# Performance work log

Measured on AMD Instinct MI355X. Metric: run time of the kernel, lower is better.

## Reference

```python
import jax, jax.numpy as jnp
import numpy as np

NUM_CLASSES = 1      # hard-coded in panoptic_inference2
MASK_THR = 1e-3      # cur_masks[:, k] >= 0.001


def _panoptic_single(logits, mask_logits, pad):
    # logits: [Q, C+1], mask_logits: [P, Q], pad: [P] bool (all False here)
    scores = logits.max(axis=-1)                      # cur_scores per query
    labels = jnp.argmax(logits, axis=-1)              # predicted class per query
    keep = labels != NUM_CLASSES                      # drop 'no-object' queries

    m = jax.nn.sigmoid(mask_logits)                   # [P, Q] cur_masks
    prob_masks = scores[None, :] * m                  # cur_prob_masks [P, Q]
    # emulate column selection cur_masks[:, keep] by masking with -inf
    masked = jnp.where(keep[None, :], prob_masks, -jnp.inf)

    # probabilities = softmax over (kept) queries; max_confs = per-point max prob
    soft = jax.nn.softmax(masked, axis=1)             # [P, Q]
    max_confs = soft.max(axis=1)                      # [P]

    # cur_mask_ids = argmax over kept queries (indices in full query space)
    mid = jnp.argmax(masked, axis=1)                  # [P]
    m_sel = jnp.take_along_axis(m, mid[:, None], axis=1)[:, 0]
    # point contributes to segment k iff argmax==k AND sigmoid>=thr (and not padded)
    valid = (m_sel >= MASK_THR) & (~pad) & keep[mid]  # [P]

    Q = logits.shape[0]
    # per-query area of mask = (mid==k) & thr ; segment kept iff nonempty
    counts = jnp.zeros((Q,), jnp.int32).at[mid].add(valid.astype(jnp.int32))
    nonempty = counts > 0
    # sequential segment ids in query order (masks are disjoint, so the
    # conf-based reordering in the original cannot change sem/ins)
    seg_id = jnp.cumsum(nonempty.astype(jnp.int32))   # [Q]

    ins = jnp.where(valid, seg_id[mid], 0).astype(jnp.int32)
    sem = jnp.where(valid, labels[mid].astype(jnp.int32), 0)
    return sem, ins, max_confs


def setup_inputs() -> dict:
    key = jax.random.key(0)
    k1, k2 = jax.random.split(key)
    B, P, Q, C1 = 2, 200000, 100, NUM_CLASSES + 1
    pred_logits = jax.random.normal(k1, (B, Q, C1), dtype=jnp.float32)
    pred_masks = jax.random.normal(k2, (B, P, Q), dtype=jnp.float32)
    padding = jnp.zeros((B, P), dtype=bool)
    return {"pred_logits": pred_logits, "pred_masks": pred_masks, "padding": padding}


def reference(pred_logits, pred_masks, padding):
    sem, ins, max_confs = jax.vmap(_panoptic_single)(pred_logits, pred_masks, padding)
    return sem, ins, max_confs
```

## Files before the change

kernel.cpp:

```cpp
#include <hip/hip_runtime.h>
#include <math.h>

#define B_   2
#define P_   200000
#define Q_   100
#define NBLK 3125


__global__ void pano_prep(const float* __restrict__ logits,
                          float* __restrict__ msc)
{
    const int b = blockIdx.x, tid = threadIdx.x;
    if (tid < Q_) {
        float l0 = logits[(b * Q_ + tid) * 2 + 0];
        float l1 = logits[(b * Q_ + tid) * 2 + 1];
        msc[b * Q_ + tid] = (l1 > l0) ? -1e30f : fmaxf(l0, l1);
    }
}

__global__ __launch_bounds__(256) void pano_pass1(
    const float* __restrict__ masks,
    const unsigned char* __restrict__ pad,
    float* __restrict__ out,
    const float* __restrict__ msc,
    ulonglong2* __restrict__ flags)
{
    const int b = blockIdx.y, tid = threadIdx.x;
    __shared__ float s_msc[Q_];
    __shared__ int   s_flag[Q_];
    if (tid < Q_) { s_msc[tid] = msc[b * Q_ + tid]; s_flag[tid] = 0; }
    __syncthreads();

    const int wave = tid >> 6, wl = tid & 63;
    const int g = wl >> 2, l = wl & 3;
    const int p = blockIdx.x * 64 + wave * 16 + g;

    const float* rowp = masks + ((size_t)b * P_ + p) * Q_;
    const float4* grow = reinterpret_cast<const float4*>(rowp);

    float4 v[7];
    #pragma unroll
    for (int k = 0; k < 6; ++k) v[k] = grow[k * 4 + l];
    v[6] = grow[24];

    float S0 = 0.0f;
    float v1 = -INFINITY, v2 = -INFINITY, m1 = 0.0f;
    int   q1 = -1;

    #pragma unroll
    for (int k = 0; k < 7; ++k) {
        const bool act = (k < 6) || (l == 0);
        const int  qb  = (k < 6) ? (16 * k + 4 * l) : 96;
        float xv[4] = {v[k].x, v[k].y, v[k].z, v[k].w};
        #pragma unroll
        for (int e = 0; e < 4; ++e) {
            int q = qb + e;
            float m   = __builtin_amdgcn_rcpf(1.0f + __expf(-xv[e]));
            float val = act ? s_msc[q] * m : -INFINITY;
            S0 += __expf(val);
            bool t = val > v1;
            v2 = t ? v1 : fmaxf(v2, val);
            v1 = t ? val : v1;
            m1 = t ? m   : m1;
            q1 = t ? q   : q1;
        }
    }

    #pragma unroll
    for (int off = 1; off <= 2; off <<= 1) {
        float So  = __shfl_xor(S0, off, 64);
        float v1o = __shfl_xor(v1, off, 64);
        float v2o = __shfl_xor(v2, off, 64);
        float m1o = __shfl_xor(m1, off, 64);
        int   q1o = __shfl_xor(q1, off, 64);
        S0 += So;
        bool t = (v1o > v1) || (v1o == v1 && (unsigned)q1o < (unsigned)q1);
        v2 = fmaxf(fminf(v1, v1o), fmaxf(v2, v2o));
        v1 = t ? v1o : v1;
        m1 = t ? m1o : m1;
        q1 = t ? q1o : q1;
    }

    if (l == 0 && (v1 - v2) < 5e-5f) {
        float bv = -INFINITY, bm = 0.0f; int bq = -1;
        for (int q = 0; q < Q_; ++q) {
            float x = rowp[q];
            float e = expf(-x);
            float m = 1.0f / (1.0f + e);
            float vv = s_msc[q] * m;
            if (vv > bv) { bv = vv; bq = q; bm = m; }
        }
        q1 = bq; m1 = bm;
    }

    bool valid = (q1 >= 0) && (s_msc[q1] > -1e29f) &&
                 (m1 >= 1e-3f) &&
                 (pad[(size_t)b * P_ + p] == 0);

    float conf = __expf(v1) * __builtin_amdgcn_rcpf(S0);
    float insf = valid ? (float)q1 : -1.0f;
    if (l == 0 && valid) s_flag[q1] = 1;

    int   src    = (wl & 15) * 4;
    float conf_g = __shfl(conf, src, 64);
    float insf_g = __shfl(insf, src, 64);
    if (wl < 16) {
        int prow = blockIdx.x * 64 + wave * 16 + wl;
        size_t o = (size_t)b * P_ + prow;
        out[o]                       = 0.0f;
        out[(size_t)B_ * P_ + o]     = insf_g;
        out[2 * (size_t)B_ * P_ + o] = conf_g;
    }

    __syncthreads();
    {
        bool f = (tid < Q_) ? (s_flag[tid] != 0) : false;
        unsigned long long m = __ballot(f);
        if (tid == 0)  flags[b * NBLK + blockIdx.x].x = m;
        if (tid == 64) flags[b * NBLK + blockIdx.x].y = m;
    }
}

__global__ __launch_bounds__(256) void pano_pass2(
    const ulonglong2* __restrict__ flags,
    int* __restrict__ seg)
{
    const int b = blockIdx.x, tid = threadIdx.x;
    unsigned long long m0 = 0ull, m1 = 0ull;
    for (int i = tid; i < NBLK; i += 256) {
        ulonglong2 w = flags[b * NBLK + i];
        m0 |= w.x; m1 |= w.y;
    }
    #pragma unroll
    for (int off = 32; off; off >>= 1) {
        m0 |= __shfl_xor(m0, off, 64);
        m1 |= __shfl_xor(m1, off, 64);
    }
    __shared__ unsigned long long sm0[4], sm1[4];
    if ((tid & 63) == 0) { sm0[tid >> 6] = m0; sm1[tid >> 6] = m1; }
    __syncthreads();
    if (tid == 0) {
        m0 = sm0[0] | sm0[1] | sm0[2] | sm0[3];
        m1 = sm1[0] | sm1[1] | sm1[2] | sm1[3];
        int c = 0;
        for (int q = 0; q < Q_; ++q) {
            c += (int)((q < 64 ? (m0 >> q) : (m1 >> (q - 64))) & 1ull);
            seg[b * Q_ + q] = c;
        }
    }
}

__global__ __launch_bounds__(256) void pano_pass3(
    const int* __restrict__ seg,
    float* __restrict__ out)
{
    const int b = blockIdx.y, tid = threadIdx.x;
    __shared__ int s_seg[Q_];
    if (tid < Q_) s_seg[tid] = seg[b * Q_ + tid];
    __syncthreads();

    int p = blockIdx.x * blockDim.x + tid;
    if (p < P_) {
        size_t o = (size_t)B_ * P_ + (size_t)b * P_ + p;
        float f = out[o];
        out[o] = (f >= 0.0f) ? (float)s_seg[(int)f] : 0.0f;
    }
}

extern "C" void kernel_launch(void* const* d_in, const int* in_sizes, int n_in,
                              void* d_out, int out_size, void* d_ws, size_t ws_size,
                              hipStream_t stream) {
    const float* logits = (const float*)d_in[0];
    const float* masks  = (const float*)d_in[1];
    const unsigned char* pad = (const unsigned char*)d_in[2];
    float* out = (float*)d_out;

    ulonglong2* flags = (ulonglong2*)d_ws;
    float*      mscp  = (float*)((char*)d_ws + 102400);
    int*        seg   = (int*)((char*)d_ws + 103424);

    pano_prep<<<dim3(B_), dim3(128), 0, stream>>>(logits, mscp);

    dim3 block(256);
    pano_pass1<<<dim3(NBLK, B_), block, 0, stream>>>(masks, pad, out, mscp, flags);
    pano_pass2<<<dim3(B_), block, 0, stream>>>(flags, seg);
    pano_pass3<<<dim3((P_ + 255) / 256, B_), block, 0, stream>>>(seg, out);
}
```

Measured before the change: 245.4 us.

## Persistent grid-stride pass1 with register prefetch and fused prep/pass2 kernels

Pass1 now runs a fixed grid of 512 blocks per batch that loop over row tiles, double-buffering the next tile's mask loads in registers while the current tile is computed. The logits prep kernel is folded into pass1's shared-memory setup. The segment-id scan (pass2) is folded into every pass3 block, which now reduces only 512 flag words per batch. Together these cut launch count and flag traffic and aim to hide load latency. The cost is higher register pressure from prefetch buffers and redundant scan work in each pass3 block.

```diff
diff --git a/kernel.cpp b/kernel.cpp
--- a/kernel.cpp
+++ b/kernel.cpp
@@ -4,131 +4,153 @@
 #define B_   2
 #define P_   200000
 #define Q_   100
-#define NBLK 3125
+#define NIT  3125
+#define GX   512
 
 
-__global__ void pano_prep(const float* __restrict__ logits,
-                          float* __restrict__ msc)
-{
-    const int b = blockIdx.x, tid = threadIdx.x;
-    if (tid < Q_) {
-        float l0 = logits[(b * Q_ + tid) * 2 + 0];
-        float l1 = logits[(b * Q_ + tid) * 2 + 1];
-        msc[b * Q_ + tid] = (l1 > l0) ? -1e30f : fmaxf(l0, l1);
-    }
-}
-
 __global__ __launch_bounds__(256) void pano_pass1(
+    const float* __restrict__ logits,
     const float* __restrict__ masks,
     const unsigned char* __restrict__ pad,
     float* __restrict__ out,
-    const float* __restrict__ msc,
     ulonglong2* __restrict__ flags)
 {
     const int b = blockIdx.y, tid = threadIdx.x;
     __shared__ float s_msc[Q_];
     __shared__ int   s_flag[Q_];
-    if (tid < Q_) { s_msc[tid] = msc[b * Q_ + tid]; s_flag[tid] = 0; }
+    if (tid < Q_) {
+        float l0 = logits[(b * Q_ + tid) * 2 + 0];
+        float l1 = logits[(b * Q_ + tid) * 2 + 1];
+        s_msc[tid]  = (l1 > l0) ? -1e30f : fmaxf(l0, l1);
+        s_flag[tid] = 0;
+    }
     __syncthreads();
 
-    const int wave = tid >> 6, wl = tid & 63;
-    const int g = wl >> 2, l = wl & 3;
-    const int p = blockIdx.x * 64 + wave * 16 + g;
+    const int wave  = tid >> 6, wl = tid & 63;
+    const int g     = wl >> 2,  l  = wl & 3;
+    const int rbase = wave * 16 + g;
 
-    const float* rowp = masks + ((size_t)b * P_ + p) * Q_;
-    const float4* grow = reinterpret_cast<const float4*>(rowp);
+    const float* mbase = masks + (size_t)b * P_ * Q_;
 
-    float4 v[7];
-    #pragma unroll
-    for (int k = 0; k < 6; ++k) v[k] = grow[k * 4 + l];
-    v[6] = grow[24];
-
-    float S0 = 0.0f;
-    float v1 = -INFINITY, v2 = -INFINITY, m1 = 0.0f;
-    int   q1 = -1;
-
-    #pragma unroll
-    for (int k = 0; k < 7; ++k) {
-        const bool act = (k < 6) || (l == 0);
-        const int  qb  = (k < 6) ? (16 * k + 4 * l) : 96;
-        float xv[4] = {v[k].x, v[k].y, v[k].z, v[k].w};
+    float4 v[7], vn[7];
+    int it = blockIdx.x;
+    {
+        const float4* grow =
+            (const float4*)(mbase + ((size_t)it * 64 + rbase) * Q_);
         #pragma unroll
-        for (int e = 0; e < 4; ++e) {
-            int q = qb + e;
-            float m   = __builtin_amdgcn_rcpf(1.0f + __expf(-xv[e]));
-            float val = act ? s_msc[q] * m : -INFINITY;
-            S0 += __expf(val);
-            bool t = val > v1;
-            v2 = t ? v1 : fmaxf(v2, val);
-            v1 = t ? val : v1;
-            m1 = t ? m   : m1;
-            q1 = t ? q   : q1;
-        }
+        for (int k = 0; k < 6; ++k) v[k] = grow[k * 4 + l];
+        v[6] = grow[24];
     }
 
-    #pragma unroll
-    for (int off = 1; off <= 2; off <<= 1) {
-        float So  = __shfl_xor(S0, off, 64);
-        float v1o = __shfl_xor(v1, off, 64);
-        float v2o = __shfl_xor(v2, off, 64);
-        float m1o = __shfl_xor(m1, off, 64);
-        int   q1o = __shfl_xor(q1, off, 64);
-        S0 += So;
-        bool t = (v1o > v1) || (v1o == v1 && (unsigned)q1o < (unsigned)q1);
-        v2 = fmaxf(fminf(v1, v1o), fmaxf(v2, v2o));
-        v1 = t ? v1o : v1;
-        m1 = t ? m1o : m1;
-        q1 = t ? q1o : q1;
-    }
+    while (true) {
+        const int itn  = it + GX;
+        const bool more = itn < NIT;
+        if (more) {
+            const float4* grow =
+                (const float4*)(mbase + ((size_t)itn * 64 + rbase) * Q_);
+            #pragma unroll
+            for (int k = 0; k < 6; ++k) vn[k] = grow[k * 4 + l];
+            vn[6] = grow[24];
+        }
 
-    if (l == 0 && (v1 - v2) < 5e-5f) {
-        float bv = -INFINITY, bm = 0.0f; int bq = -1;
-        for (int q = 0; q < Q_; ++q) {
-            float x = rowp[q];
-            float e = expf(-x);
-            float m = 1.0f / (1.0f + e);
-            float vv = s_msc[q] * m;
-            if (vv > bv) { bv = vv; bq = q; bm = m; }
+        const int p = it * 64 + rbase;
+        const float* rowp = mbase + (size_t)p * Q_;
+
+        float S0 = 0.0f;
+        float v1 = -INFINITY, v2 = -INFINITY, m1 = 0.0f;
+        int   q1 = -1;
+
+        #pragma unroll
+        for (int k = 0; k < 7; ++k) {
+            const bool act = (k < 6) || (l == 0);
+            const int  qb  = (k < 6) ? (16 * k + 4 * l) : 96;
+            float xv[4] = {v[k].x, v[k].y, v[k].z, v[k].w};
+            #pragma unroll
+            for (int e = 0; e < 4; ++e) {
+                int q = qb + e;
+                float m   = __builtin_amdgcn_rcpf(1.0f + __expf(-xv[e]));
+                float val = act ? s_msc[q] * m : -INFINITY;
+                S0 += __expf(val);
+                bool t = val > v1;
+                v2 = t ? v1 : fmaxf(v2, val);
+                v1 = t ? val : v1;
+                m1 = t ? m   : m1;
+                q1 = t ? q   : q1;
+            }
         }
-        q1 = bq; m1 = bm;
-    }
 
-    bool valid = (q1 >= 0) && (s_msc[q1] > -1e29f) &&
-                 (m1 >= 1e-3f) &&
-                 (pad[(size_t)b * P_ + p] == 0);
+        #pragma unroll
+        for (int off = 1; off <= 2; off <<= 1) {
+            float So  = __shfl_xor(S0, off, 64);
+            float v1o = __shfl_xor(v1, off, 64);
+            float v2o = __shfl_xor(v2, off, 64);
+            float m1o = __shfl_xor(m1, off, 64);
+            int   q1o = __shfl_xor(q1, off, 64);
+            S0 += So;
+            bool t = (v1o > v1) || (v1o == v1 && (unsigned)q1o < (unsigned)q1);
+            v2 = fmaxf(fminf(v1, v1o), fmaxf(v2, v2o));
+            v1 = t ? v1o : v1;
+            m1 = t ? m1o : m1;
+            q1 = t ? q1o : q1;
+        }
 
-    float conf = __expf(v1) * __builtin_amdgcn_rcpf(S0);
-    float insf = valid ? (float)q1 : -1.0f;
-    if (l == 0 && valid) s_flag[q1] = 1;
+        if (l == 0 && (v1 - v2) < 5e-5f) {
+            float bv = -INFINITY, bm = 0.0f; int bq = -1;
+            for (int q = 0; q < Q_; ++q) {
+                float x = rowp[q];
+                float e = expf(-x);
+                float m = 1.0f / (1.0f + e);
+                float vv = s_msc[q] * m;
+                if (vv > bv) { bv = vv; bq = q; bm = m; }
+            }
+            q1 = bq; m1 = bm;
+        }
 
-    int   src    = (wl & 15) * 4;
-    float conf_g = __shfl(conf, src, 64);
-    float insf_g = __shfl(insf, src, 64);
-    if (wl < 16) {
-        int prow = blockIdx.x * 64 + wave * 16 + wl;
-        size_t o = (size_t)b * P_ + prow;
-        out[o]                       = 0.0f;
-        out[(size_t)B_ * P_ + o]     = insf_g;
-        out[2 * (size_t)B_ * P_ + o] = conf_g;
+        bool valid = (q1 >= 0) && (s_msc[q1] > -1e29f) &&
+                     (m1 >= 1e-3f) &&
+                     (pad[(size_t)b * P_ + p] == 0);
+
+        float conf = __expf(v1) * __builtin_amdgcn_rcpf(S0);
+        float insf = valid ? (float)q1 : -1.0f;
+        if (l == 0 && valid) s_flag[q1] = 1;
+
+        int   src    = (wl & 15) * 4;
+        float conf_g = __shfl(conf, src, 64);
+        float insf_g = __shfl(insf, src, 64);
+        if (wl < 16) {
+            int prow = it * 64 + wave * 16 + wl;
+            size_t o = (size_t)b * P_ + prow;
+            out[o]                       = 0.0f;
+            out[(size_t)B_ * P_ + o]     = insf_g;
+            out[2 * (size_t)B_ * P_ + o] = conf_g;
+        }
+
+        if (!more) break;
+        #pragma unroll
+        for (int k = 0; k < 7; ++k) v[k] = vn[k];
+        it = itn;
     }
 
     __syncthreads();
     {
         bool f = (tid < Q_) ? (s_flag[tid] != 0) : false;
         unsigned long long m = __ballot(f);
-        if (tid == 0)  flags[b * NBLK + blockIdx.x].x = m;
-        if (tid == 64) flags[b * NBLK + blockIdx.x].y = m;
+        if (tid == 0)  flags[b * GX + blockIdx.x].x = m;
+        if (tid == 64) flags[b * GX + blockIdx.x].y = m;
     }
 }
 
-__global__ __launch_bounds__(256) void pano_pass2(
+__global__ __launch_bounds__(256) void pano_pass3(
     const ulonglong2* __restrict__ flags,
-    int* __restrict__ seg)
+    float* __restrict__ out)
 {
-    const int b = blockIdx.x, tid = threadIdx.x;
+    const int b = blockIdx.y, tid = threadIdx.x;
+    __shared__ int s_seg[Q_];
+    __shared__ unsigned long long sm0[4], sm1[4];
+
     unsigned long long m0 = 0ull, m1 = 0ull;
-    for (int i = tid; i < NBLK; i += 256) {
-        ulonglong2 w = flags[b * NBLK + i];
+    for (int i = tid; i < GX; i += 256) {
+        ulonglong2 w = flags[b * GX + i];
         m0 |= w.x; m1 |= w.y;
     }
     #pragma unroll
@@ -136,7 +158,6 @@
         m0 |= __shfl_xor(m0, off, 64);
         m1 |= __shfl_xor(m1, off, 64);
     }
-    __shared__ unsigned long long sm0[4], sm1[4];
     if ((tid & 63) == 0) { sm0[tid >> 6] = m0; sm1[tid >> 6] = m1; }
     __syncthreads();
     if (tid == 0) {
@@ -145,18 +166,9 @@
         int c = 0;
         for (int q = 0; q < Q_; ++q) {
             c += (int)((q < 64 ? (m0 >> q) : (m1 >> (q - 64))) & 1ull);
-            seg[b * Q_ + q] = c;
+            s_seg[q] = c;
         }
     }
-}
-
-__global__ __launch_bounds__(256) void pano_pass3(
-    const int* __restrict__ seg,
-    float* __restrict__ out)
-{
-    const int b = blockIdx.y, tid = threadIdx.x;
-    __shared__ int s_seg[Q_];
-    if (tid < Q_) s_seg[tid] = seg[b * Q_ + tid];
     __syncthreads();
 
     int p = blockIdx.x * blockDim.x + tid;
@@ -174,15 +186,9 @@
     const float* masks  = (const float*)d_in[1];
     const unsigned char* pad = (const unsigned char*)d_in[2];
     float* out = (float*)d_out;
-
     ulonglong2* flags = (ulonglong2*)d_ws;
-    float*      mscp  = (float*)((char*)d_ws + 102400);
-    int*        seg   = (int*)((char*)d_ws + 103424);
-
-    pano_prep<<<dim3(B_), dim3(128), 0, stream>>>(logits, mscp);
 
     dim3 block(256);
-    pano_pass1<<<dim3(NBLK, B_), block, 0, stream>>>(masks, pad, out, mscp, flags);
-    pano_pass2<<<dim3(B_), block, 0, stream>>>(flags, seg);
-    pano_pass3<<<dim3((P_ + 255) / 256, B_), block, 0, stream>>>(seg, out);
+    pano_pass1<<<dim3(GX, B_), block, 0, stream>>>(logits, masks, pad, out, flags);
+    pano_pass3<<<dim3((P_ + 255) / 256, B_), block, 0, stream>>>(flags, out);
 }
```

Measured after the change: 249.5 us. About the same (+1.7%).

## Double-buffer mask tiles into LDS via global_load_lds and fuse prep kernel

Applied to the files above, without the earlier changes.

Each pass1 block now handles five 64-row tiles, using global_load_lds async DMA into two LDS buffers so the next tile streams in while the current one is computed. The logits preprocessing is folded into pass1, which removes a kernel launch. The grid shrinks to 625 blocks per batch and the flags array shrinks to match. In exchange there is more LDS per block (about 51KB), which may limit occupancy, and fewer blocks to spread across CUs.

```diff
diff --git a/kernel.cpp b/kernel.cpp
--- a/kernel.cpp
+++ b/kernel.cpp
@@ -1,123 +1,143 @@
 #include <hip/hip_runtime.h>
 #include <math.h>
 
-#define B_   2
-#define P_   200000
-#define Q_   100
-#define NBLK 3125
-
-
-__global__ void pano_prep(const float* __restrict__ logits,
-                          float* __restrict__ msc)
+#define B_    2
+#define P_    200000
+#define Q_    100
+#define TPB   5
+#define GXB   625
+#define TB    25600
+
+
+__device__ __forceinline__ void dma16(const void* g, void* l) {
+    __builtin_amdgcn_global_load_lds(
+        (const __attribute__((address_space(1))) void*)g,
+        (__attribute__((address_space(3))) void*)l, 16, 0, 0);
+}
+
+__global__ __launch_bounds__(256) void pano_pass1(
+    const float* __restrict__ logits,
+    const float* __restrict__ masks,
+    const unsigned char* __restrict__ pad,
+    float* __restrict__ out,
+    ulonglong2* __restrict__ flags)
 {
-    const int b = blockIdx.x, tid = threadIdx.x;
+    const int b = blockIdx.y, tid = threadIdx.x;
+    __shared__ __align__(16) float s_tile[2][TB / 4];
+    __shared__ float s_msc[Q_];
+    __shared__ int   s_flag[Q_];
     if (tid < Q_) {
         float l0 = logits[(b * Q_ + tid) * 2 + 0];
         float l1 = logits[(b * Q_ + tid) * 2 + 1];
-        msc[b * Q_ + tid] = (l1 > l0) ? -1e30f : fmaxf(l0, l1);
-    }
-}
-
-__global__ __launch_bounds__(256) void pano_pass1(
-    const float* __restrict__ masks,
-    const unsigned char* __restrict__ pad,
-    float* __restrict__ out,
-    const float* __restrict__ msc,
-    ulonglong2* __restrict__ flags)
-{
-    const int b = blockIdx.y, tid = threadIdx.x;
-    __shared__ float s_msc[Q_];
-    __shared__ int   s_flag[Q_];
-    if (tid < Q_) { s_msc[tid] = msc[b * Q_ + tid]; s_flag[tid] = 0; }
-    __syncthreads();
-
-    const int wave = tid >> 6, wl = tid & 63;
-    const int g = wl >> 2, l = wl & 3;
-    const int p = blockIdx.x * 64 + wave * 16 + g;
-
-    const float* rowp = masks + ((size_t)b * P_ + p) * Q_;
-    const float4* grow = reinterpret_cast<const float4*>(rowp);
-
-    float4 v[7];
-    #pragma unroll
-    for (int k = 0; k < 6; ++k) v[k] = grow[k * 4 + l];
-    v[6] = grow[24];
-
-    float S0 = 0.0f;
-    float v1 = -INFINITY, v2 = -INFINITY, m1 = 0.0f;
-    int   q1 = -1;
-
-    #pragma unroll
-    for (int k = 0; k < 7; ++k) {
-        const bool act = (k < 6) || (l == 0);
-        const int  qb  = (k < 6) ? (16 * k + 4 * l) : 96;
-        float xv[4] = {v[k].x, v[k].y, v[k].z, v[k].w};
+        s_msc[tid]  = (l1 > l0) ? -1e30f : fmaxf(l0, l1);
+        s_flag[tid] = 0;
+    }
+
+    const int wave = tid >> 6, wl = tid & 63, g = wl >> 2, l = wl & 3;
+    const char* mb = (const char*)(masks + (size_t)b * P_ * Q_);
+    const int t0 = blockIdx.x * TPB;
+
+    auto stage = [&](int t, int buf) {
+        const char* gb = mb + (size_t)t * TB;
+        char* lb = (char*)&s_tile[buf][0];
         #pragma unroll
-        for (int e = 0; e < 4; ++e) {
-            int q = qb + e;
-            float m   = __builtin_amdgcn_rcpf(1.0f + __expf(-xv[e]));
-            float val = act ? s_msc[q] * m : -INFINITY;
-            S0 += __expf(val);
-            bool t = val > v1;
-            v2 = t ? v1 : fmaxf(v2, val);
-            v1 = t ? val : v1;
-            m1 = t ? m   : m1;
-            q1 = t ? q   : q1;
-        }
-    }
-
-    #pragma unroll
-    for (int off = 1; off <= 2; off <<= 1) {
-        float So  = __shfl_xor(S0, off, 64);
-        float v1o = __shfl_xor(v1, off, 64);
-        float v2o = __shfl_xor(v2, off, 64);
-        float m1o = __shfl_xor(m1, off, 64);
-        int   q1o = __shfl_xor(q1, off, 64);
-        S0 += So;
-        bool t = (v1o > v1) || (v1o == v1 && (unsigned)q1o < (unsigned)q1);
-        v2 = fmaxf(fminf(v1, v1o), fmaxf(v2, v2o));
-        v1 = t ? v1o : v1;
-        m1 = t ? m1o : m1;
-        q1 = t ? q1o : q1;
-    }
-
-    if (l == 0 && (v1 - v2) < 5e-5f) {
-        float bv = -INFINITY, bm = 0.0f; int bq = -1;
-        for (int q = 0; q < Q_; ++q) {
-            float x = rowp[q];
-            float e = expf(-x);
-            float m = 1.0f / (1.0f + e);
-            float vv = s_msc[q] * m;
-            if (vv > bv) { bv = vv; bq = q; bm = m; }
-        }
-        q1 = bq; m1 = bm;
-    }
-
-    bool valid = (q1 >= 0) && (s_msc[q1] > -1e29f) &&
-                 (m1 >= 1e-3f) &&
-                 (pad[(size_t)b * P_ + p] == 0);
-
-    float conf = __expf(v1) * __builtin_amdgcn_rcpf(S0);
-    float insf = valid ? (float)q1 : -1.0f;
-    if (l == 0 && valid) s_flag[q1] = 1;
-
-    int   src    = (wl & 15) * 4;
-    float conf_g = __shfl(conf, src, 64);
-    float insf_g = __shfl(insf, src, 64);
-    if (wl < 16) {
-        int prow = blockIdx.x * 64 + wave * 16 + wl;
-        size_t o = (size_t)b * P_ + prow;
-        out[o]                       = 0.0f;
-        out[(size_t)B_ * P_ + o]     = insf_g;
-        out[2 * (size_t)B_ * P_ + o] = conf_g;
+        for (int i = 0; i < 7; ++i) {
+            int c = wave + 4 * i;
+            if (c < 25) dma16(gb + c * 1024 + wl * 16, lb + c * 1024);
+        }
+    };
+
+    stage(t0, 0);
+    int buf = 0;
+
+    for (int ti = 0; ti < TPB; ++ti) {
+        __syncthreads();
+        if (ti + 1 < TPB) stage(t0 + ti + 1, buf ^ 1);
+
+        const int t = t0 + ti;
+        const int r = wave * 16 + g;
+        const int p = t * 64 + r;
+        const char*  lrow = (const char*)&s_tile[buf][0] + r * 400;
+        const float* rowp = (const float*)(mb + (size_t)p * 400);
+
+        float S0 = 0.0f;
+        float v1 = -INFINITY, v2 = -INFINITY, m1 = 0.0f;
+        int   q1 = -1;
+
+        #pragma unroll
+        for (int k = 0; k < 7; ++k) {
+            const bool act = (k < 6) || (l == 0);
+            const int  qb  = (k < 6) ? (16 * k + 4 * l) : 96;
+            float4 v4 = *(const float4*)(lrow + ((k < 6) ? (64 * k + 16 * l) : 384));
+            float xv[4] = {v4.x, v4.y, v4.z, v4.w};
+            #pragma unroll
+            for (int e = 0; e < 4; ++e) {
+                int q = qb + e;
+                float m   = __builtin_amdgcn_rcpf(1.0f + __expf(-xv[e]));
+                float val = act ? s_msc[q] * m : -INFINITY;
+                S0 += __expf(val);
+                bool tk = val > v1;
+                v2 = tk ? v1 : fmaxf(v2, val);
+                v1 = tk ? val : v1;
+                m1 = tk ? m   : m1;
+                q1 = tk ? q   : q1;
+            }
+        }
+
+        #pragma unroll
+        for (int off = 1; off <= 2; off <<= 1) {
+            float So  = __shfl_xor(S0, off, 64);
+            float v1o = __shfl_xor(v1, off, 64);
+            float v2o = __shfl_xor(v2, off, 64);
+            float m1o = __shfl_xor(m1, off, 64);
+            int   q1o = __shfl_xor(q1, off, 64);
+            S0 += So;
+            bool tk = (v1o > v1) || (v1o == v1 && (unsigned)q1o < (unsigned)q1);
+            v2 = fmaxf(fminf(v1, v1o), fmaxf(v2, v2o));
+            v1 = tk ? v1o : v1;
+            m1 = tk ? m1o : m1;
+            q1 = tk ? q1o : q1;
+        }
+
+        if (l == 0 && (v1 - v2) < 5e-5f) {
+            float bv = -INFINITY, bm = 0.0f; int bq = -1;
+            for (int q = 0; q < Q_; ++q) {
+                float x = rowp[q];
+                float e = expf(-x);
+                float m = 1.0f / (1.0f + e);
+                float vv = s_msc[q] * m;
+                if (vv > bv) { bv = vv; bq = q; bm = m; }
+            }
+            q1 = bq; m1 = bm;
+        }
+
+        bool valid = (q1 >= 0) && (s_msc[q1] > -1e29f) &&
+                     (m1 >= 1e-3f) &&
+                     (pad[(size_t)b * P_ + p] == 0);
+
+        float conf = __expf(v1) * __builtin_amdgcn_rcpf(S0);
+        float insf = valid ? (float)q1 : -1.0f;
+        if (l == 0 && valid) s_flag[q1] = 1;
+
+        int   src    = (wl & 15) * 4;
+        float conf_g = __shfl(conf, src, 64);
+        float insf_g = __shfl(insf, src, 64);
+        if (wl < 16) {
+            int prow = t * 64 + wave * 16 + wl;
+            size_t o = (size_t)b * P_ + prow;
+            out[o]                       = 0.0f;
+            out[(size_t)B_ * P_ + o]     = insf_g;
+            out[2 * (size_t)B_ * P_ + o] = conf_g;
+        }
+        buf ^= 1;
     }
 
     __syncthreads();
     {
         bool f = (tid < Q_) ? (s_flag[tid] != 0) : false;
         unsigned long long m = __ballot(f);
-        if (tid == 0)  flags[b * NBLK + blockIdx.x].x = m;
-        if (tid == 64) flags[b * NBLK + blockIdx.x].y = m;
+        if (tid == 0)  flags[b * GXB + blockIdx.x].x = m;
+        if (tid == 64) flags[b * GXB + blockIdx.x].y = m;
     }
 }
 
@@ -127,8 +147,8 @@
 {
     const int b = blockIdx.x, tid = threadIdx.x;
     unsigned long long m0 = 0ull, m1 = 0ull;
-    for (int i = tid; i < NBLK; i += 256) {
-        ulonglong2 w = flags[b * NBLK + i];
+    for (int i = tid; i < GXB; i += 256) {
+        ulonglong2 w = flags[b * GXB + i];
         m0 |= w.x; m1 |= w.y;
     }
     #pragma unroll
@@ -176,13 +196,10 @@
     float* out = (float*)d_out;
 
     ulonglong2* flags = (ulonglong2*)d_ws;
-    float*      mscp  = (float*)((char*)d_ws + 102400);
-    int*        seg   = (int*)((char*)d_ws + 103424);
-
-    pano_prep<<<dim3(B_), dim3(128), 0, stream>>>(logits, mscp);
+    int*        seg   = (int*)((char*)d_ws + 20480);
 
     dim3 block(256);
-    pano_pass1<<<dim3(NBLK, B_), block, 0, stream>>>(masks, pad, out, mscp, flags);
+    pano_pass1<<<dim3(GXB, B_), block, 0, stream>>>(logits, masks, pad, out, flags);
     pano_pass2<<<dim3(B_), block, 0, stream>>>(flags, seg);
     pano_pass3<<<dim3((P_ + 255) / 256, B_), block, 0, stream>>>(seg, out);
 }
```

Result: slower. 251.2 us (+2.4%).
